# Kernel optimization log

Measured on AMD Instinct MI355X. Metric: run time of the kernel, lower is better.

Reference implementation:

```python
import jax, jax.numpy as jnp
import numpy as np

THRESHOLD = 0.5
NEG_POS = 3
ALPHA = 0.5
EPS = 1e-6


def cxcy2xy(b):
    return jnp.concatenate([b[:, :2] - b[:, 2:] / 2, b[:, :2] + b[:, 2:] / 2], axis=1)


def xy2cxcy(b):
    return jnp.concatenate([(b[:, 2:] + b[:, :2]) / 2, b[:, 2:] - b[:, :2]], axis=1)


def encode_boxes(b, d):
    return jnp.concatenate([(b[:, :2] - d[:, :2]) / (d[:, 2:] / 10 + EPS),
                            jnp.log(b[:, 2:] / d[:, 2:] + EPS) * 5], axis=1)


def find_iou(a, b):
    # a: [O,4] xy, b: [N,4] xy -> [O,N]
    lt = jnp.maximum(a[:, None, :2], b[None, :, :2])
    rb = jnp.minimum(a[:, None, 2:], b[None, :, 2:])
    wh = jnp.clip(rb - lt, 0.0)
    inter = wh[..., 0] * wh[..., 1]
    area_a = (a[:, 2] - a[:, 0]) * (a[:, 3] - a[:, 1])
    area_b = (b[:, 2] - b[:, 0]) * (b[:, 3] - b[:, 1])
    return inter / (area_a[:, None] + area_b[None, :] - inter)


def _match(boxes_i, labels_i, def_xy, default_boxes):
    # boxes_i: [O,4] xy, labels_i: [O], def_xy/default_boxes: [N,4]
    n_obj = boxes_i.shape[0]
    overlap = find_iou(boxes_i, def_xy)            # [O, N]
    overlap_defbox = overlap.max(axis=0)           # [N]
    object_defbox = overlap.argmax(axis=0)         # [N]
    defbox_object = overlap.argmax(axis=1)         # [O]
    object_defbox = object_defbox.at[defbox_object].set(jnp.arange(n_obj))
    overlap_defbox = overlap_defbox.at[defbox_object].set(1.0)
    label = labels_i[object_defbox]
    label = jnp.where(overlap_defbox < THRESHOLD, 0, label)
    t_loc = encode_boxes(xy2cxcy(boxes_i[object_defbox]), default_boxes)
    return t_loc, label


def reference(locs_pred, cls_pred, boxes, labels, default_boxes):
    B, N, C = cls_pred.shape
    def_xy = cxcy2xy(default_boxes)
    t_locs, t_classes = jax.vmap(_match, in_axes=(0, 0, None, None))(
        boxes, labels, def_xy, default_boxes)      # [B,N,4], [B,N]

    pos = t_classes != 0                            # [B,N]
    n_pos = pos.sum(axis=1)                         # [B]
    n_pos_total = n_pos.sum().astype(jnp.float32)

    # SmoothL1 (beta=1), mean over positive-box coordinate elements
    d = jnp.abs(locs_pred - t_locs)
    sl1 = jnp.where(d < 1.0, 0.5 * d * d, d - 0.5)
    loc_loss = jnp.sum(sl1 * pos[..., None].astype(sl1.dtype)) / (n_pos_total * 4.0)

    # per-anchor cross entropy
    logp = jax.nn.log_softmax(cls_pred, axis=-1)
    all_conf = -jnp.take_along_axis(logp, t_classes[..., None], axis=-1)[..., 0]  # [B,N]

    pos_conf = jnp.sum(jnp.where(pos, all_conf, 0.0))
    neg_conf = jnp.where(pos, 0.0, all_conf)
    neg_sorted = -jnp.sort(-neg_conf, axis=1)       # descending
    hard = jnp.arange(N)[None, :] < (NEG_POS * n_pos)[:, None]
    hard_sum = jnp.sum(jnp.where(hard, neg_sorted, 0.0))

    conf_loss = (hard_sum + pos_conf) / n_pos_total
    return ALPHA * loc_loss + conf_loss


def setup_inputs() -> dict:
    key = jax.random.key(0)
    k1, k2, k3, k4, k5, k6, k7 = jax.random.split(key, 7)
    B, N, C, O = 32, 24564, 81, 16
    locs_pred = jax.random.normal(k1, (B, N, 4), dtype=jnp.float32)
    cls_pred = jax.random.normal(k2, (B, N, C), dtype=jnp.float32)
    # ground-truth boxes: valid xy boxes inside [0,1]
    cxy = jax.random.uniform(k3, (B, O, 2), minval=0.2, maxval=0.8)
    wh = jax.random.uniform(k4, (B, O, 2), minval=0.05, maxval=0.3)
    boxes = jnp.concatenate([cxy - wh / 2, cxy + wh / 2], axis=-1).astype(jnp.float32)
    labels = jax.random.randint(k5, (B, O), 1, C)
    dcxy = jax.random.uniform(k6, (N, 2), minval=0.05, maxval=0.95)
    dwh = jax.random.uniform(k7, (N, 2), minval=0.05, maxval=0.4)
    default_boxes = jnp.concatenate([dcxy, dwh], axis=-1).astype(jnp.float32)
    return {"locs_pred": locs_pred, "cls_pred": cls_pred, "boxes": boxes,
            "labels": labels, "default_boxes": default_boxes}
```

## Files before the change

### kernel.cpp

```cpp
#include <hip/hip_runtime.h>
#include <math.h>

#define THRESH    0.5f
#define NEG_POSK  3
#define EPSf      1e-6f
#define CCLS      81
#define TILEA     64
#define CHUNKS    16
#define TPB       16

__device__ __forceinline__ float iou_xy(float ax0, float ay0, float ax1, float ay1,
                                        float bx0, float by0, float bx1, float by1) {
    float lx = fmaxf(ax0, bx0), ly = fmaxf(ay0, by0);
    float rx = fminf(ax1, bx1), ry = fminf(ay1, by1);
    float w = fmaxf(rx - lx, 0.f), h = fmaxf(ry - ly, 0.f);
    float inter = w * h;
    float aa = (ax1 - ax0) * (ay1 - ay0);
    float ab = (bx1 - bx0) * (by1 - by0);
    return inter / (aa + ab - inter);
}

__device__ __forceinline__ void gload16(const void* g, void* l) {
    __builtin_amdgcn_global_load_lds(
        (const __attribute__((address_space(1))) void*)g,
        (__attribute__((address_space(3))) void*)l, 16, 0, 0);
}

__global__ __launch_bounds__(256) void k_obj_part(const float* __restrict__ boxes,
                                                  const float* __restrict__ dboxes,
                                                  float* __restrict__ part_iou,
                                                  int* __restrict__ part_idx,
                                                  int N, int O) {
    int bo = blockIdx.x;
    int c  = blockIdx.y;
    const float* bb = boxes + (size_t)bo * 4;
    float ax0 = bb[0], ay0 = bb[1], ax1 = bb[2], ay1 = bb[3];
    int chunk = (N + CHUNKS - 1) / CHUNKS;
    int n0 = c * chunk;
    int n1 = min(n0 + chunk, N);
    float best = -1.f; int bi = 0x7FFFFFFF;
    for (int n = n0 + threadIdx.x; n < n1; n += 256) {
        float4 d = ((const float4*)dboxes)[n];
        float dx0 = d.x - d.z * 0.5f, dy0 = d.y - d.w * 0.5f;
        float dx1 = d.x + d.z * 0.5f, dy1 = d.y + d.w * 0.5f;
        float iou = iou_xy(ax0, ay0, ax1, ay1, dx0, dy0, dx1, dy1);
        if (iou > best) { best = iou; bi = n; }
    }
    #pragma unroll
    for (int dd = 1; dd < 64; dd <<= 1) {
        float v2 = __shfl_xor(best, dd); int i2 = __shfl_xor(bi, dd);
        if (v2 > best || (v2 == best && i2 < bi)) { best = v2; bi = i2; }
    }
    __shared__ float sv[4]; __shared__ int si[4];
    int w = threadIdx.x >> 6;
    if ((threadIdx.x & 63) == 0) { sv[w] = best; si[w] = bi; }
    __syncthreads();
    if (threadIdx.x == 0) {
        #pragma unroll
        for (int i = 1; i < 4; ++i)
            if (sv[i] > best || (sv[i] == best && si[i] < bi)) { best = sv[i]; bi = si[i]; }
        part_iou[(size_t)bo * CHUNKS + c] = best;
        part_idx[(size_t)bo * CHUNKS + c] = bi;
    }
}

__global__ void k_obj_reduce(const float* __restrict__ part_iou,
                             const int* __restrict__ part_idx,
                             int* __restrict__ defbox_object, int BO) {
    int bo = blockIdx.x * blockDim.x + threadIdx.x;
    if (bo >= BO) return;
    float best = -1.f; int bi = 0x7FFFFFFF;
    #pragma unroll
    for (int c = 0; c < CHUNKS; ++c) {
        float v = part_iou[(size_t)bo * CHUNKS + c];
        int  i = part_idx[(size_t)bo * CHUNKS + c];
        if (v > best || (v == best && i < bi)) { best = v; bi = i; }
    }
    defbox_object[bo] = bi;
}

template<int OT>
__global__ __launch_bounds__(256)
void k_conf(const float* __restrict__ locs_pred,
            const float* __restrict__ cls,
            const float* __restrict__ boxes,
            const int* __restrict__ labels,
            const float* __restrict__ dboxes,
            const int* __restrict__ dbo_g,
            float* __restrict__ vneg,
            int* __restrict__ n_pos,
            float* __restrict__ loc_sum,
            float* __restrict__ pos_conf,
            int N, int O_rt, int bpb, int tilesPerBatch, long long maxF4) {
    const int O = OT ? OT : O_rt;
    __shared__ __align__(16) float sm[4][2][16 * CCLS];
    __shared__ float sbb[64];
    __shared__ int slab[16], sdbo[16];
    __shared__ float swl[4], swp[4];
    __shared__ int swc[4];
    const int tid = threadIdx.x;
    const int b  = blockIdx.x / bpb;
    const int t0 = (blockIdx.x % bpb) * TPB;
    const int tEnd = min(t0 + TPB, tilesPerBatch);

    if (tid < O * 4) sbb[tid] = boxes[(size_t)b * O * 4 + tid];
    else if (tid < O * 5) slab[tid - O * 4] = labels[(size_t)b * O + tid - O * 4];
    else if (tid < O * 6) sdbo[tid - O * 5] = dbo_g[(size_t)b * O + tid - O * 5];

    const int lane = tid & 63, w = tid >> 6;
    const int j = lane & 15, q = lane >> 4;

    auto stage = [&](int buf, int t) {
        long long base4 = (((long long)b * N + (long long)t * TILEA + w * 16)
                           * CCLS) >> 2;
        const float4* g4 = (const float4*)cls;
        float4* s4 = (float4*)&sm[w][buf][0];
        #pragma unroll
        for (int k2 = 0; k2 < 5; ++k2) {
            long long gi = base4 + k2 * 64 + lane;
            if (gi > maxF4) gi = maxF4;
            gload16(g4 + gi, s4 + k2 * 64);
        }
        if (lane < 4) {
            long long gi = base4 + 320 + lane;
            if (gi > maxF4) gi = maxF4;
            gload16(g4 + gi, s4 + 320);
        }
    };

    stage(0, t0);
    __syncthreads();

    float obx0[4], oby0[4], obx1[4], oby1[4], oarea[4];
    int odbo[4];
    #pragma unroll
    for (int oo = 0; oo < 4; ++oo) {
        int o = q * 4 + oo;
        obx0[oo] = sbb[o*4];   oby0[oo] = sbb[o*4+1];
        obx1[oo] = sbb[o*4+2]; oby1[oo] = sbb[o*4+3];
        oarea[oo] = (obx1[oo] - obx0[oo]) * (oby1[oo] - oby0[oo]);
        odbo[oo] = sdbo[o];
    }

    float pc = 0.f, ls = 0.f; int cnt = 0;

    auto phase2 = [&](int buf, int t) {
        int a0 = t * TILEA;
        int valid = min(TILEA, N - a0);
        int a = w * 16 + j;
        bool act = a < valid;
        int n = a0 + a;
        int nc = min(n, N - 1);
        float4 d = ((const float4*)dboxes)[nc];
        float dx0 = d.x - d.z * 0.5f, dy0 = d.y - d.w * 0.5f;
        float dx1 = d.x + d.z * 0.5f, dy1 = d.y + d.w * 0.5f;
        float areaD = d.z * d.w;
        float bi = -1.f, bu = 1.f; int bsel = q * 4;
        int fs = -1;
        #pragma unroll
        for (int oo = 0; oo < 4; ++oo) {
            float lx = fmaxf(obx0[oo], dx0), ly = fmaxf(oby0[oo], dy0);
            float rx = fminf(obx1[oo], dx1), ry = fminf(oby1[oo], dy1);
            float ww = fmaxf(rx - lx, 0.f), hh = fmaxf(ry - ly, 0.f);
            float inter = ww * hh;
            float uni = oarea[oo] + areaD - inter;
            float c1 = inter * bu, c2 = bi * uni;
            if (c1 > c2) { bi = inter; bu = uni; bsel = q * 4 + oo; }
            if (odbo[oo] == n) fs = q * 4 + oo;
        }
        #pragma unroll
        for (int dd = 16; dd < 64; dd <<= 1) {
            float oi = __shfl_xor(bi, dd), ou = __shfl_xor(bu, dd);
            int os = __shfl_xor(bsel, dd);
            int of = __shfl_xor(fs, dd);
            float c1 = oi * bu, c2 = bi * ou;
            if (c1 > c2 || (c1 == c2 && os < bsel)) { bi = oi; bu = ou; bsel = os; }
            fs = max(fs, of);
        }
        const float* row = &sm[w][buf][j * CCLS];
        float s_ = 0.f;
        if (act) {
            int c0 = q * 20;
            float e0 = 0.f, e1 = 0.f, e2 = 0.f, e3 = 0.f;
            #pragma unroll
            for (int i = 0; i < 20; i += 4) {
                e0 += __expf(row[c0 + i]);
                e1 += __expf(row[c0 + i + 1]);
                e2 += __expf(row[c0 + i + 2]);
                e3 += __expf(row[c0 + i + 3]);
            }
            s_ = (e0 + e1) + (e2 + e3);
            if (q == 3) s_ += __expf(row[80]);
        }
        s_ += __shfl_xor(s_, 16);
        s_ += __shfl_xor(s_, 32);
        if (act && q == 0) {
            bool forced = fs >= 0;
            int sel = forced ? fs : bsel;
            bool meets = forced || (bi >= 0.5f * bu);
            int lbl = meets ? slab[sel] : 0;
            float conf = __logf(s_) - row[lbl];
            bool pos = (lbl != 0);
            size_t idx = (size_t)b * N + n;
            float4 p = ((const float4*)locs_pred)[idx];
            vneg[idx] = pos ? 0.f : conf;
            if (pos) {
                pc += conf; cnt++;
                float bx0 = sbb[sel*4], by0 = sbb[sel*4+1];
                float bx1 = sbb[sel*4+2], by1 = sbb[sel*4+3];
                float bcx = (bx0 + bx1) * 0.5f, bcy = (by0 + by1) * 0.5f;
                float bw = bx1 - bx0, bh = by1 - by0;
                float t0f = (bcx - d.x) / (d.z / 10.0f + EPSf);
                float t1f = (bcy - d.y) / (d.w / 10.0f + EPSf);
                float t2f = __logf(bw / d.z + EPSf) * 5.0f;
                float t3f = __logf(bh / d.w + EPSf) * 5.0f;
                float dd;
                dd = fabsf(p.x - t0f); ls += (dd < 1.f) ? 0.5f*dd*dd : dd - 0.5f;
                dd = fabsf(p.y - t1f); ls += (dd < 1.f) ? 0.5f*dd*dd : dd - 0.5f;
                dd = fabsf(p.z - t2f); ls += (dd < 1.f) ? 0.5f*dd*dd : dd - 0.5f;
                dd = fabsf(p.w - t3f); ls += (dd < 1.f) ? 0.5f*dd*dd : dd - 0.5f;
            }
        }
    };

    int cur = 0;
    for (int t = t0; t < tEnd; ++t) {
        bool has_next = (t + 1 < tEnd);
        if (has_next) stage(cur ^ 1, t + 1);
        if (t == t0)
            asm volatile("s_waitcnt vmcnt(6)" ::: "memory");
        else if (has_next)
            asm volatile("s_waitcnt vmcnt(9)" ::: "memory");
        else
            asm volatile("s_waitcnt vmcnt(3)" ::: "memory");
        phase2(cur, t);
        cur ^= 1;
    }

    #pragma unroll
    for (int dd = 1; dd < 64; dd <<= 1) {
        pc  += __shfl_xor(pc, dd);
        ls  += __shfl_xor(ls, dd);
        cnt += __shfl_xor(cnt, dd);
    }
    if (lane == 0) { swp[w] = pc; swl[w] = ls; swc[w] = cnt; }
    __syncthreads();
    if (tid == 0) {
        float P = swp[0] + swp[1] + swp[2] + swp[3];
        float L = swl[0] + swl[1] + swl[2] + swl[3];
        int   C = swc[0] + swc[1] + swc[2] + swc[3];
        if (C) {
            atomicAdd(&n_pos[b], C);
            atomicAdd(loc_sum, L);
            atomicAdd(pos_conf, P);
        }
    }
}

__device__ void wave_select(const int* hist, int nbins, int k, int* out_bin, int* out_k) {
    int lane = threadIdx.x & 63;
    int cum = 0;
    for (int c = nbins / 64 - 1; c >= 0; --c) {
        int val = hist[c * 64 + lane];
        int s = val;
        for (int d = 1; d < 64; d <<= 1) {
            int t = __shfl_down(s, d);
            if (lane + d < 64) s += t;
        }
        int total = __shfl(s, 0);
        if (cum + total >= k) {
            unsigned long long mask = __ballot(cum + s >= k);
            int bl = 63 - __builtin_clzll(mask);
            int sB = __shfl(s, bl);
            int vB = __shfl(val, bl);
            if (lane == 0) {
                *out_bin = c * 64 + bl;
                *out_k = k - (cum + sB - vB);
            }
            return;
        }
        cum += total;
    }
    if (lane == 0) { *out_bin = 0; *out_k = 1; }
}

__global__ __launch_bounds__(1024) void k_select(const float* __restrict__ vneg,
                                                 const int* __restrict__ n_pos,
                                                 float* __restrict__ hard_sum,
                                                 int B, int N) {
    int b = blockIdx.x;
    const float* v = vneg + (size_t)b * N;
    __shared__ int hist[2048];
    __shared__ int bcast_bin, bcast_k;
    __shared__ float swv[16];
    __shared__ int swc[16];
    int np = n_pos[b];
    long long kk = (long long)NEG_POSK * np;
    if (kk > N) kk = N;
    int k = (int)kk;
    if (k <= 0) return;
    int tid = threadIdx.x;

    for (int i = tid; i < 2048; i += 1024) hist[i] = 0;
    __syncthreads();
    for (int n = tid; n < N; n += 1024) {
        unsigned u = __float_as_uint(v[n]);
        atomicAdd(&hist[u >> 20], 1);
    }
    __syncthreads();
    if (tid < 64) wave_select(hist, 2048, k, &bcast_bin, &bcast_k);
    __syncthreads();
    int B1 = bcast_bin, k2 = bcast_k;

    for (int i = tid; i < 2048; i += 1024) hist[i] = 0;
    __syncthreads();
    for (int n = tid; n < N; n += 1024) {
        unsigned u = __float_as_uint(v[n]);
        if ((int)(u >> 20) == B1) atomicAdd(&hist[(u >> 9) & 0x7FF], 1);
    }
    __syncthreads();
    if (tid < 64) wave_select(hist, 2048, k2, &bcast_bin, &bcast_k);
    __syncthreads();
    int B2 = bcast_bin, k3 = bcast_k;
    unsigned pre = ((unsigned)B1 << 11) | (unsigned)B2;

    for (int i = tid; i < 512; i += 1024) hist[i] = 0;
    __syncthreads();
    for (int n = tid; n < N; n += 1024) {
        unsigned u = __float_as_uint(v[n]);
        if ((u >> 9) == pre) atomicAdd(&hist[u & 0x1FF], 1);
    }
    __syncthreads();
    if (tid < 64) wave_select(hist, 512, k3, &bcast_bin, &bcast_k);
    __syncthreads();
    unsigned tau_bits = (pre << 9) | (unsigned)bcast_bin;
    float tau = __uint_as_float(tau_bits);

    float ssum = 0.f; int scnt = 0;
    for (int n = tid; n < N; n += 1024) {
        float x = v[n];
        if (x > tau) { ssum += x; scnt++; }
    }
    for (int d = 1; d < 64; d <<= 1) {
        ssum += __shfl_xor(ssum, d);
        scnt += __shfl_xor(scnt, d);
    }
    int w = tid >> 6;
    if ((tid & 63) == 0) { swv[w] = ssum; swc[w] = scnt; }
    __syncthreads();
    if (tid == 0) {
        float S = 0.f; int Ct = 0;
        for (int i = 0; i < 16; ++i) { S += swv[i]; Ct += swc[i]; }
        float hb = S + (float)(k - Ct) * tau;
        atomicAdd(hard_sum, hb);
    }
}

__global__ void k_final(const int* __restrict__ n_pos,
                        const float* __restrict__ loc_sum,
                        const float* __restrict__ pos_conf,
                        const float* __restrict__ hard_sum,
                        float* __restrict__ out, int B) {
    if (threadIdx.x == 0 && blockIdx.x == 0) {
        int tot = 0;
        for (int b = 0; b < B; ++b) tot += n_pos[b];
        float np = (float)tot;
        float loc = *loc_sum / (np * 4.0f);
        float conf = (*hard_sum + *pos_conf) / np;
        out[0] = 0.5f * loc + conf;
    }
}

extern "C" void kernel_launch(void* const* d_in, const int* in_sizes, int n_in,
                              void* d_out, int out_size, void* d_ws, size_t ws_size,
                              hipStream_t stream) {
    const float* locs_pred = (const float*)d_in[0];
    const float* cls_pred  = (const float*)d_in[1];
    const float* boxes     = (const float*)d_in[2];
    const int*   labels    = (const int*)d_in[3];
    const float* dboxes    = (const float*)d_in[4];

    int N = in_sizes[4] / 4;
    int B = in_sizes[0] / (4 * N);
    int O = in_sizes[3] / B;
    int BO = B * O;

    size_t BN = (size_t)B * N;
    char* ws = (char*)d_ws;
    int*   n_pos    = (int*)ws;
    float* loc_sum  = (float*)(ws + 128);
    float* pos_conf = (float*)(ws + 132);
    float* hard_sum = (float*)(ws + 136);
    float* vneg     = (float*)(ws + 256);
    int*   defbox_object = (int*)(ws + 256 + BN * 4);
    float* part_iou = (float*)(ws + 256 + BN * 4 + (size_t)BO * 4);
    int*   part_idx = (int*)(part_iou + (size_t)BO * CHUNKS);

    hipMemsetAsync(ws, 0, 256, stream);

    dim3 gop(BO, CHUNKS);
    k_obj_part<<<gop, 256, 0, stream>>>(boxes, dboxes, part_iou, part_idx, N, O);
    k_obj_reduce<<<(BO + 255) / 256, 256, 0, stream>>>(part_iou, part_idx,
                                                       defbox_object, BO);
    int tilesPerBatch = (N + TILEA - 1) / TILEA;
    int bpb = (tilesPerBatch + TPB - 1) / TPB;
    long long maxF4 = (((long long)B * N * CCLS) >> 2) - 1;
    dim3 gc(B * bpb);
    if (O == 16)
        k_conf<16><<<gc, 256, 0, stream>>>(locs_pred, cls_pred, boxes, labels, dboxes,
                                           defbox_object, vneg, n_pos, loc_sum,
                                           pos_conf, N, O, bpb, tilesPerBatch, maxF4);
    else
        k_conf<0><<<gc, 256, 0, stream>>>(locs_pred, cls_pred, boxes, labels, dboxes,
                                          defbox_object, vneg, n_pos, loc_sum,
                                          pos_conf, N, O, bpb, tilesPerBatch, maxF4);
    k_select<<<B, 1024, 0, stream>>>(vneg, n_pos, hard_sum, B, N);
    k_final<<<1, 1, 0, stream>>>(n_pos, loc_sum, pos_conf, hard_sum, (float*)d_out, B);
}
```

Baseline: 124.8 us.

## Software-pipeline LDS-to-register loads of class rows ahead of the matching compute

Restructures the per-tile loop into a register double-buffered pipeline. The next tile's class-logit row is read from LDS into registers while the current tile's IoU matching runs. That frees the LDS buffer early, so the global-to-LDS stage for tile t+2 can be issued sooner. It also gathers the target logit across lanes with shuffles instead of an indexed LDS read, and issues the locs_pred load early. The cost is more register pressure and hand-tuned vmcnt/lgkmcnt waits that are fragile; the vmcnt counts assume each stage issues a fixed number of loads per lane.

After: 130.3 us. 4.4% more time.

```diff
diff --git a/kernel.cpp b/kernel.cpp
--- a/kernel.cpp
+++ b/kernel.cpp
@@ -128,6 +128,15 @@
         }
     };
 
+    auto loadRegs = [&](float (&RR)[20], float& R80, int bufIdx) {
+        const float* rowp = &sm[w][bufIdx][j * CCLS];
+        __builtin_amdgcn_sched_barrier(0);
+        #pragma unroll
+        for (int i = 0; i < 20; ++i) RR[i] = rowp[q * 20 + i];
+        R80 = rowp[80];
+        __builtin_amdgcn_sched_barrier(0);
+    };
+
     stage(0, t0);
     __syncthreads();
 
@@ -144,17 +153,22 @@
 
     float pc = 0.f, ls = 0.f; int cnt = 0;
 
-    auto phase2 = [&](int buf, int t) {
+    struct MRes { float4 d, p; int lbl, sel, n; bool act; };
+
+    auto matchTile = [&](int t) -> MRes {
+        MRes m;
         int a0 = t * TILEA;
-        int valid = min(TILEA, N - a0);
         int a = w * 16 + j;
-        bool act = a < valid;
-        int n = a0 + a;
-        int nc = min(n, N - 1);
-        float4 d = ((const float4*)dboxes)[nc];
-        float dx0 = d.x - d.z * 0.5f, dy0 = d.y - d.w * 0.5f;
-        float dx1 = d.x + d.z * 0.5f, dy1 = d.y + d.w * 0.5f;
-        float areaD = d.z * d.w;
+        m.n = a0 + a;
+        m.act = m.n < N;
+        int nc = min(m.n, N - 1);
+        size_t idx = (size_t)b * N + nc;
+        m.d = ((const float4*)dboxes)[nc];
+        m.p = make_float4(0.f, 0.f, 0.f, 0.f);
+        if (q == 0) m.p = ((const float4*)locs_pred)[idx];
+        float dx0 = m.d.x - m.d.z * 0.5f, dy0 = m.d.y - m.d.w * 0.5f;
+        float dx1 = m.d.x + m.d.z * 0.5f, dy1 = m.d.y + m.d.w * 0.5f;
+        float areaD = m.d.z * m.d.w;
         float bi = -1.f, bu = 1.f; int bsel = q * 4;
         int fs = -1;
         #pragma unroll
@@ -166,7 +180,7 @@
             float uni = oarea[oo] + areaD - inter;
             float c1 = inter * bu, c2 = bi * uni;
             if (c1 > c2) { bi = inter; bu = uni; bsel = q * 4 + oo; }
-            if (odbo[oo] == n) fs = q * 4 + oo;
+            if (odbo[oo] == m.n) fs = q * 4 + oo;
         }
         #pragma unroll
         for (int dd = 16; dd < 64; dd <<= 1) {
@@ -177,64 +191,87 @@
             if (c1 > c2 || (c1 == c2 && os < bsel)) { bi = oi; bu = ou; bsel = os; }
             fs = max(fs, of);
         }
-        const float* row = &sm[w][buf][j * CCLS];
-        float s_ = 0.f;
-        if (act) {
-            int c0 = q * 20;
-            float e0 = 0.f, e1 = 0.f, e2 = 0.f, e3 = 0.f;
-            #pragma unroll
-            for (int i = 0; i < 20; i += 4) {
-                e0 += __expf(row[c0 + i]);
-                e1 += __expf(row[c0 + i + 1]);
-                e2 += __expf(row[c0 + i + 2]);
-                e3 += __expf(row[c0 + i + 3]);
-            }
-            s_ = (e0 + e1) + (e2 + e3);
-            if (q == 3) s_ += __expf(row[80]);
-        }
+        bool forced = fs >= 0;
+        m.sel = forced ? fs : bsel;
+        bool meets = forced || (bi >= 0.5f * bu);
+        m.lbl = meets ? slab[m.sel] : 0;
+        return m;
+    };
+
+    auto expStore = [&](const float (&RR)[20], float R80, const MRes& m) {
+        float e0 = 0.f, e1 = 0.f, e2 = 0.f, e3 = 0.f;
+        #pragma unroll
+        for (int i = 0; i < 20; i += 4) {
+            e0 += __expf(RR[i]);     e1 += __expf(RR[i + 1]);
+            e2 += __expf(RR[i + 2]); e3 += __expf(RR[i + 3]);
+        }
+        float s_ = (e0 + e1) + (e2 + e3);
+        if (q == 3) s_ += __expf(R80);
+        float xl = (m.lbl == 80 && q == 3) ? R80 : 0.f;
+        #pragma unroll
+        for (int i = 0; i < 20; ++i)
+            if (q * 20 + i == m.lbl) xl = RR[i];
         s_ += __shfl_xor(s_, 16);
+        xl += __shfl_xor(xl, 16);
         s_ += __shfl_xor(s_, 32);
-        if (act && q == 0) {
-            bool forced = fs >= 0;
-            int sel = forced ? fs : bsel;
-            bool meets = forced || (bi >= 0.5f * bu);
-            int lbl = meets ? slab[sel] : 0;
-            float conf = __logf(s_) - row[lbl];
-            bool pos = (lbl != 0);
-            size_t idx = (size_t)b * N + n;
-            float4 p = ((const float4*)locs_pred)[idx];
+        xl += __shfl_xor(xl, 32);
+        if (m.act && q == 0) {
+            float conf = __logf(s_) - xl;
+            bool pos = (m.lbl != 0);
+            size_t idx = (size_t)b * N + m.n;
             vneg[idx] = pos ? 0.f : conf;
             if (pos) {
                 pc += conf; cnt++;
+                int sel = m.sel;
                 float bx0 = sbb[sel*4], by0 = sbb[sel*4+1];
                 float bx1 = sbb[sel*4+2], by1 = sbb[sel*4+3];
                 float bcx = (bx0 + bx1) * 0.5f, bcy = (by0 + by1) * 0.5f;
                 float bw = bx1 - bx0, bh = by1 - by0;
-                float t0f = (bcx - d.x) / (d.z / 10.0f + EPSf);
-                float t1f = (bcy - d.y) / (d.w / 10.0f + EPSf);
-                float t2f = __logf(bw / d.z + EPSf) * 5.0f;
-                float t3f = __logf(bh / d.w + EPSf) * 5.0f;
-                float dd;
-                dd = fabsf(p.x - t0f); ls += (dd < 1.f) ? 0.5f*dd*dd : dd - 0.5f;
-                dd = fabsf(p.y - t1f); ls += (dd < 1.f) ? 0.5f*dd*dd : dd - 0.5f;
-                dd = fabsf(p.z - t2f); ls += (dd < 1.f) ? 0.5f*dd*dd : dd - 0.5f;
-                dd = fabsf(p.w - t3f); ls += (dd < 1.f) ? 0.5f*dd*dd : dd - 0.5f;
+                float t0f = (bcx - m.d.x) / (m.d.z / 10.0f + EPSf);
+                float t1f = (bcy - m.d.y) / (m.d.w / 10.0f + EPSf);
+                float t2f = __logf(bw / m.d.z + EPSf) * 5.0f;
+                float t3f = __logf(bh / m.d.w + EPSf) * 5.0f;
+                float dd2;
+                dd2 = fabsf(m.p.x - t0f); ls += (dd2 < 1.f) ? 0.5f*dd2*dd2 : dd2 - 0.5f;
+                dd2 = fabsf(m.p.y - t1f); ls += (dd2 < 1.f) ? 0.5f*dd2*dd2 : dd2 - 0.5f;
+                dd2 = fabsf(m.p.z - t2f); ls += (dd2 < 1.f) ? 0.5f*dd2*dd2 : dd2 - 0.5f;
+                dd2 = fabsf(m.p.w - t3f); ls += (dd2 < 1.f) ? 0.5f*dd2*dd2 : dd2 - 0.5f;
             }
         }
     };
 
-    int cur = 0;
-    for (int t = t0; t < tEnd; ++t) {
-        bool has_next = (t + 1 < tEnd);
-        if (has_next) stage(cur ^ 1, t + 1);
-        if (t == t0)
-            asm volatile("s_waitcnt vmcnt(6)" ::: "memory");
-        else if (has_next)
-            asm volatile("s_waitcnt vmcnt(9)" ::: "memory");
-        else
-            asm volatile("s_waitcnt vmcnt(3)" ::: "memory");
-        phase2(cur, t);
-        cur ^= 1;
+    float rrA[20], r80A, rrB[20], r80B;
+    loadRegs(rrA, r80A, 0);
+    stage(1, t0 + 1);
+
+    int t = t0;
+    #pragma unroll 1
+    for (int half = 0; half < TPB / 2; ++half) {
+        {
+            bool hasNext = (t + 1 < tEnd);
+            if (hasNext) {
+                if (t == t0) asm volatile("s_waitcnt vmcnt(0)" ::: "memory");
+                else         asm volatile("s_waitcnt vmcnt(1)" ::: "memory");
+                loadRegs(rrB, r80B, (t + 1 - t0) & 1);
+            }
+            MRes m = matchTile(t);
+            asm volatile("s_waitcnt lgkmcnt(0)" ::: "memory");
+            if (t + 2 < tEnd) stage((t - t0) & 1, t + 2);
+            expStore(rrA, r80A, m);
+        }
+        ++t; if (t >= tEnd) break;
+        {
+            bool hasNext = (t + 1 < tEnd);
+            if (hasNext) {
+                asm volatile("s_waitcnt vmcnt(1)" ::: "memory");
+                loadRegs(rrA, r80A, (t + 1 - t0) & 1);
+            }
+            MRes m = matchTile(t);
+            asm volatile("s_waitcnt lgkmcnt(0)" ::: "memory");
+            if (t + 2 < tEnd) stage((t - t0) & 1, t + 2);
+            expStore(rrB, r80B, m);
+        }
+        ++t; if (t >= tEnd) break;
     }
 
     #pragma unroll
```
